# Kernel optimization log

Measured on AMD Instinct MI355X. Metric: run time of the kernel, lower is better.

The kernel has to match this reference:

```python
import jax, jax.numpy as jnp
import numpy as np

B, CI, CO = 16, 16, 16
M1, M2, M3 = 6, 6, 6
NT, NX, NY = 39, 28, 28
NXr, NYr = 14, 14  # int((n-1)/2 + 1) for n=28


def setup_inputs() -> dict:
    key = jax.random.key(0)
    ks = jax.random.split(key, 9)
    scale = 1.0 / (CI * CO)
    u = lambda k, s: scale * jax.random.uniform(k, s, dtype=jnp.float32)
    return {
        "x": jax.random.normal(ks[0], (B, CI, NT, NXr, NYr), dtype=jnp.float32),
        "wp1_re": u(ks[1], (CI, CO, M1)), "wp1_im": u(ks[2], (CI, CO, M1)),
        "wp2_re": u(ks[3], (CI, CO, M2)), "wp2_im": u(ks[4], (CI, CO, M2)),
        "wp3_re": u(ks[5], (CI, CO, M3)), "wp3_im": u(ks[6], (CI, CO, M3)),
        "wr_re": u(ks[7], (CI, CO, M1, M2, M3)), "wr_im": u(ks[8], (CI, CO, M1, M2, M3)),
    }


def _forward(x, wp1, wp2, wp3, wr):
    # grids (match torch.linspace with hardcoded nt/nx/ny and truncation)
    tt_np = np.linspace(0.0, NT - 1, NT)
    tx_np = np.linspace(0.0, 1.0, NX)[:NXr]
    ty_np = np.linspace(0.0, 1.0, NY)[:NYr]
    dtt = float(tt_np[1] - tt_np[0])
    dtx = float(tx_np[1] - tx_np[0])
    dty = float(ty_np[1] - ty_np[0])

    alpha = jnp.fft.fftn(x, axes=(-3, -2, -1))  # [B, CI, NT, NXr, NYr] complex64

    lam1 = (2j * np.pi * jnp.fft.fftfreq(NT, dtt)).astype(jnp.complex64)   # [NT]
    lam2 = (2j * np.pi * jnp.fft.fftfreq(NXr, dtx)).astype(jnp.complex64)  # [NXr]
    lam3 = (2j * np.pi * jnp.fft.fftfreq(NYr, dty)).astype(jnp.complex64)  # [NYr]

    # per-axis pole reciprocals: 1/((l1-p1)(l2-p2)(l3-p3)) = (1/(l1-p1))(1/(l2-p2))(1/(l3-p3))
    r1 = 1.0 / (lam1[:, None, None, None] - wp1[None])  # [NT,  CI, CO, M1]
    r2 = 1.0 / (lam2[:, None, None, None] - wp2[None])  # [NXr, CI, CO, M2]
    r3 = 1.0 / (lam3[:, None, None, None] - wp3[None])  # [NYr, CI, CO, M3]

    # Hw[m,n,l,i,k,p,q,r] = wr[i,k,p,q,r]*r1[m,i,k,p]*r2[n,i,k,q]*r3[l,i,k,r]
    # output_residue1[b,k,m,n,l] = sum_{i,p,q,r} alpha[b,i,m,n,l] * Hw
    or1 = jnp.einsum('bimnl,ikpqr,mikp,nikq,likr->bkmnl', alpha, wr, r1, r2, r3)
    # output_residue2[b,k,p,q,r] = -sum_{i,m,n,l} alpha[b,i,m,n,l] * Hw
    or2 = -jnp.einsum('bimnl,ikpqr,mikp,nikq,likr->bkpqr', alpha, wr, r1, r2, r3)

    x1 = jnp.real(jnp.fft.ifftn(or1, s=(NT, NXr, NYr), axes=(-3, -2, -1))).astype(jnp.float32)

    tt = jnp.asarray(tt_np, dtype=jnp.float32).astype(jnp.complex64)
    tx = jnp.asarray(tx_np, dtype=jnp.float32).astype(jnp.complex64)
    ty = jnp.asarray(ty_np, dtype=jnp.float32).astype(jnp.complex64)

    e1 = jnp.exp(wp1[..., None] * tt)  # [CI, CO, M1, NT]
    e2 = jnp.exp(wp2[..., None] * tx)  # [CI, CO, M2, NXr]
    e3 = jnp.exp(wp3[..., None] * ty)  # [CI, CO, M3, NYr]

    # x2[k,i,z,x,y] = Re( sum_{b,p,q,m} or2[k,b,p,q,m]*e1[b,i,p,z]*e2[b,i,q,x]*e3[b,i,m,y] )
    x2 = jnp.real(jnp.einsum('kbpqm,bipz,biqx,bimy->kizxy', or2, e1, e2, e3)).astype(jnp.float32)
    x2 = x2 / (NT * NXr * NYr)
    return x1 + x2


def reference(x, wp1_re, wp1_im, wp2_re, wp2_im, wp3_re, wp3_im, wr_re, wr_im):
    wp1 = jax.lax.complex(wp1_re, wp1_im)
    wp2 = jax.lax.complex(wp2_re, wp2_im)
    wp3 = jax.lax.complex(wp3_re, wp3_im)
    wr = jax.lax.complex(wr_re, wr_im)
    return _forward(x, wp1, wp2, wp3, wr)
```

## Files before the change

### kernel.cpp

```cpp
#include <hip/hip_runtime.h>

constexpr int kB  = 16;
constexpr int kC  = 16;
constexpr int kM  = 6;
constexpr int kNT = 39;
constexpr int kNX = 14;
constexpr int kNY = 14;
constexpr int kNS = kNX * kNY;
constexpr int kNF = kNT * kNS;
constexpr int kNIK = kC * kC;
constexpr int kMR = kM * kM * kM;
constexpr int kFCH = 6;

__device__ __forceinline__ float2 cmul(float2 a, float2 b) {
    return make_float2(a.x * b.x - a.y * b.y, a.x * b.y + a.y * b.x);
}
__device__ __forceinline__ void cfma(float2& c, float2 a, float2 b) {
    c.x = fmaf(a.x, b.x, fmaf(-a.y, b.y, c.x));
    c.y = fmaf(a.x, b.y, fmaf(a.y, b.x, c.y));
}

__global__ __launch_bounds__(256) void k_init(
    const float* __restrict__ wp1_re, const float* __restrict__ wp1_im,
    const float* __restrict__ wp2_re, const float* __restrict__ wp2_im,
    const float* __restrict__ wp3_re, const float* __restrict__ wp3_im,
    float2* __restrict__ F39, float2* __restrict__ F14,
    float2* __restrict__ r1t, float2* __restrict__ r2t, float2* __restrict__ r3t,
    float2* __restrict__ e1t, float2* __restrict__ e2t, float2* __restrict__ e3t)
{
    const float PI2 = 6.283185307179586f;
    int tid = blockIdx.x * blockDim.x + threadIdx.x;
    int nth = gridDim.x * blockDim.x;

    for (int idx = tid; idx < kNT * kNT; idx += nth) {
        int m = idx / kNT, t = idx % kNT;
        float ang = -PI2 * (float)((m * t) % kNT) / (float)kNT;
        float s, c; sincosf(ang, &s, &c);
        F39[idx] = make_float2(c, s);
    }
    for (int idx = tid; idx < kNX * kNX; idx += nth) {
        int a = idx / kNX, b = idx % kNX;
        float ang = -PI2 * (float)((a * b) % kNX) / (float)kNX;
        float s, c; sincosf(ang, &s, &c);
        F14[idx] = make_float2(c, s);
    }
    for (int idx = tid; idx < kNIK * kM * kNT; idx += nth) {
        int z = idx % kNT; int ikp = idx / kNT;
        float wre = wp1_re[ikp], wim = wp1_im[ikp];
        float f = (z < 20 ? (float)z : (float)(z - kNT)) / (float)kNT;
        float w = PI2 * f;
        float dr = -wre, di = w - wim;
        float inv = 1.0f / (dr * dr + di * di);
        r1t[idx] = make_float2(dr * inv, -di * inv);
        float tt = (float)z;
        float er = expf(wre * tt);
        float s, c; sincosf(wim * tt, &s, &c);
        e1t[idx] = make_float2(er * c, er * s);
    }
    for (int idx = tid; idx < kNIK * kM * kNX; idx += nth) {
        int n = idx % kNX; int ikq = idx / kNX;
        float f = (n <= 6 ? (float)n : (float)(n - kNX)) * 27.0f / 14.0f;
        float w = PI2 * f;
        float tx = (float)n * (1.0f / 27.0f);
        {
            float wre = wp2_re[ikq], wim = wp2_im[ikq];
            float dr = -wre, di = w - wim;
            float inv = 1.0f / (dr * dr + di * di);
            r2t[idx] = make_float2(dr * inv, -di * inv);
            float er = expf(wre * tx);
            float s, c; sincosf(wim * tx, &s, &c);
            e2t[idx] = make_float2(er * c, er * s);
        }
        {
            float wre = wp3_re[ikq], wim = wp3_im[ikq];
            float dr = -wre, di = w - wim;
            float inv = 1.0f / (dr * dr + di * di);
            r3t[idx] = make_float2(dr * inv, -di * inv);
            float er = expf(wre * tx);
            float s, c; sincosf(wim * tx, &s, &c);
            e3t[idx] = make_float2(er * c, er * s);
        }
    }
}

__global__ __launch_bounds__(256) void k_dft_t_real(
    const float* __restrict__ x, const float2* __restrict__ F39, float2* __restrict__ out)
{
    int bc = blockIdx.x, mg = blockIdx.y;
    __shared__ float2 Fs[13 * kNT];
    int t = threadIdx.x;
    for (int j = t; j < 13 * kNT; j += 256)
        Fs[j] = F39[(mg * 13 + j / kNT) * kNT + (j % kNT)];
    __syncthreads();
    if (t < kNS) {
        float col[kNT];
        const float* xp = x + (size_t)bc * kNF + t;
        #pragma unroll
        for (int tt = 0; tt < kNT; ++tt) col[tt] = xp[(size_t)tt * kNS];
        for (int mi = 0; mi < 13; ++mi) {
            float2 acc = make_float2(0.f, 0.f);
            #pragma unroll
            for (int tt = 0; tt < kNT; ++tt) {
                float2 f = Fs[mi * kNT + tt];
                acc.x = fmaf(f.x, col[tt], acc.x);
                acc.y = fmaf(f.y, col[tt], acc.y);
            }
            out[((size_t)bc * kNT + mg * 13 + mi) * kNS + t] = acc;
        }
    }
}

__global__ __launch_bounds__(256) void k_idft_t(
    const float2* __restrict__ in, const float2* __restrict__ F39, float2* __restrict__ out)
{
    int bk = blockIdx.x, zg = blockIdx.y;
    __shared__ float2 Fs[13 * kNT];
    int t = threadIdx.x;
    for (int j = t; j < 13 * kNT; j += 256) {
        float2 f = F39[(zg * 13 + j / kNT) * kNT + (j % kNT)];
        f.y = -f.y;
        Fs[j] = f;
    }
    __syncthreads();
    if (t < kNS) {
        float2 col[kNT];
        const float2* ip = in + (size_t)bk * kNF + t;
        #pragma unroll
        for (int m = 0; m < kNT; ++m) col[m] = ip[(size_t)m * kNS];
        for (int zi = 0; zi < 13; ++zi) {
            float2 acc = make_float2(0.f, 0.f);
            #pragma unroll
            for (int m = 0; m < kNT; ++m) cfma(acc, Fs[zi * kNT + m], col[m]);
            out[((size_t)bk * kNT + zg * 13 + zi) * kNS + t] = acc;
        }
    }
}

__global__ __launch_bounds__(256) void k_dft_xy(
    const float2* __restrict__ in, const float2* __restrict__ F14, float2* __restrict__ out)
{
    int bm = blockIdx.x;
    __shared__ float2 tile[kNS];
    __shared__ float2 tmp[kNS];
    __shared__ float2 Fs[kNX * kNX];
    int t = threadIdx.x;
    if (t < kNS) tile[t] = in[(size_t)bm * kNS + t];
    if (t < kNX * kNX) Fs[t] = F14[t];
    __syncthreads();
    if (t < kNS) {
        int n2 = t / kNY, l = t % kNY;
        float2 acc = make_float2(0.f, 0.f);
        #pragma unroll
        for (int n = 0; n < kNX; ++n) cfma(acc, Fs[n2 * kNX + n], tile[n * kNY + l]);
        tmp[t] = acc;
    }
    __syncthreads();
    if (t < kNS) {
        int n = t / kNY, l2 = t % kNY;
        float2 acc = make_float2(0.f, 0.f);
        #pragma unroll
        for (int l = 0; l < kNY; ++l) cfma(acc, Fs[l2 * kNY + l], tmp[n * kNY + l]);
        out[(size_t)bm * kNS + t] = acc;
    }
}

__global__ __launch_bounds__(256) void k_idft_xy_final(
    const float2* __restrict__ in, const float2* __restrict__ F14, float* __restrict__ outp)
{
    int bm = blockIdx.x;
    __shared__ float2 tile[kNS];
    __shared__ float2 tmp[kNS];
    __shared__ float2 Fs[kNX * kNX];
    int t = threadIdx.x;
    if (t < kNS) tile[t] = in[(size_t)bm * kNS + t];
    if (t < kNX * kNX) { float2 f = F14[t]; f.y = -f.y; Fs[t] = f; }
    __syncthreads();
    if (t < kNS) {
        int n2 = t / kNY, l = t % kNY;
        float2 acc = make_float2(0.f, 0.f);
        #pragma unroll
        for (int n = 0; n < kNX; ++n) cfma(acc, Fs[n2 * kNX + n], tile[n * kNY + l]);
        tmp[t] = acc;
    }
    __syncthreads();
    if (t < kNS) {
        int n = t / kNY, l2 = t % kNY;
        float2 acc = make_float2(0.f, 0.f);
        #pragma unroll
        for (int l = 0; l < kNY; ++l) cfma(acc, Fs[l2 * kNY + l], tmp[n * kNY + l]);
        outp[(size_t)bm * kNS + t] += acc.x * (1.0f / 7644.0f);
    }
}

__global__ __launch_bounds__(256) void k_H(
    const float* __restrict__ wr_re, const float* __restrict__ wr_im,
    const float2* __restrict__ r1t, const float2* __restrict__ r2t,
    const float2* __restrict__ r3t, float2* __restrict__ H)
{
    int ik = blockIdx.x;
    __shared__ float2 wrs[kMR];
    __shared__ float2 r1s[kM * kNT];
    __shared__ float2 r2s[kM * kNX];
    __shared__ float2 r3s[kM * kNY];
    __shared__ float2 As[kM * kM * kNY];
    __shared__ float2 Ss[kM * kNS];
    int t = threadIdx.x;
    for (int j = t; j < kMR; j += 256)
        wrs[j] = make_float2(wr_re[ik * kMR + j], wr_im[ik * kMR + j]);
    for (int j = t; j < kM * kNT; j += 256) r1s[j] = r1t[(size_t)ik * kM * kNT + j];
    for (int j = t; j < kM * kNX; j += 256) r2s[j] = r2t[(size_t)ik * kM * kNX + j];
    for (int j = t; j < kM * kNY; j += 256) r3s[j] = r3t[(size_t)ik * kM * kNY + j];
    __syncthreads();
    for (int j = t; j < kM * kM * kNY; j += 256) {
        int l = j % kNY; int pq = j / kNY;
        float2 acc = make_float2(0.f, 0.f);
        #pragma unroll
        for (int r = 0; r < kM; ++r) cfma(acc, wrs[pq * kM + r], r3s[r * kNY + l]);
        As[j] = acc;
    }
    __syncthreads();
    for (int j = t; j < kM * kNS; j += 256) {
        int l = j % kNY; int n = (j / kNY) % kNX; int p = j / kNS;
        float2 acc = make_float2(0.f, 0.f);
        #pragma unroll
        for (int q = 0; q < kM; ++q) cfma(acc, r2s[q * kNX + n], As[(p * kM + q) * kNY + l]);
        Ss[j] = acc;
    }
    __syncthreads();
    for (int j = t; j < kNF; j += 256) {
        int m = j / kNS; int nl = j % kNS;
        float2 acc = make_float2(0.f, 0.f);
        #pragma unroll
        for (int p = 0; p < kM; ++p) cfma(acc, r1s[p * kNT + m], Ss[p * kNS + nl]);
        H[(size_t)ik * kNF + j] = acc;
    }
}

__global__ __launch_bounds__(256) void k_or1(
    const float2* __restrict__ alpha, const float2* __restrict__ H, float2* __restrict__ out)
{
    int f0 = blockIdx.x * kFCH;
    __shared__ float2 As[256 * 7 + 16];
    __shared__ float2 Hs[256 * 7 + 16];
    int t = threadIdx.x;
    {
        const float2* ap = alpha + (size_t)t * kNF + f0;
        const float2* hp = H + (size_t)t * kNF + f0;
        int base = t * 7 + (t >> 4);
        #pragma unroll
        for (int j = 0; j < kFCH; ++j) {
            As[base + j] = ap[j];
            Hs[base + j] = hp[j];
        }
    }
    __syncthreads();
    int b = t >> 4, k = t & 15;
    float2 acc[kFCH];
    #pragma unroll
    for (int j = 0; j < kFCH; ++j) acc[j] = make_float2(0.f, 0.f);
    #pragma unroll
    for (int i = 0; i < kC; ++i) {
        int ai = (b * 16 + i) * 7 + b;
        int hi = (i * 16 + k) * 7 + i;
        #pragma unroll
        for (int j = 0; j < kFCH; ++j) cfma(acc[j], As[ai + j], Hs[hi + j]);
    }
    float2* op = out + (size_t)t * kNF + f0;
    #pragma unroll
    for (int j = 0; j < kFCH; ++j) op[j] = acc[j];
}

__global__ __launch_bounds__(256) void k_or2p(
    const float2* __restrict__ alpha,
    const float* __restrict__ wr_re, const float* __restrict__ wr_im,
    const float2* __restrict__ r1t, const float2* __restrict__ r2t,
    const float2* __restrict__ r3t, float2* __restrict__ P)
{
    int blk = blockIdx.x;
    int i = blk % kC; int rest = blk / kC;
    int k = rest % kC; int pb = rest / kC;
    int b0 = 2 * pb, b1 = 2 * pb + 1;
    int ik = i * kC + k;
    __shared__ float2 r1s[kM * kNT];
    __shared__ float2 r2s[kM * kNX];
    __shared__ float2 r3s[kM * kNY];
    __shared__ float2 wrs[kMR];
    __shared__ float2 T1a[kM * kNS];
    __shared__ float2 T1b[kM * kNS];
    __shared__ float2 T2a[kM * kM * kNY];
    __shared__ float2 T2b[kM * kM * kNY];
    int t = threadIdx.x;
    for (int j = t; j < kM * kNT; j += 256) r1s[j] = r1t[(size_t)ik * kM * kNT + j];
    for (int j = t; j < kM * kNX; j += 256) r2s[j] = r2t[(size_t)ik * kM * kNX + j];
    for (int j = t; j < kM * kNY; j += 256) r3s[j] = r3t[(size_t)ik * kM * kNY + j];
    for (int j = t; j < kMR; j += 256)
        wrs[j] = make_float2(wr_re[ik * kMR + j], wr_im[ik * kMR + j]);
    __syncthreads();
    if (t < kNS) {
        float2 c0 = make_float2(0.f, 0.f), c1 = c0, c2 = c0, c3 = c0, c4 = c0, c5 = c0;
        float2 d0 = c0, d1 = c0, d2 = c0, d3 = c0, d4 = c0, d5 = c0;
        const float2* ap0 = alpha + (size_t)(b0 * kC + i) * kNF + t;
        const float2* ap1 = alpha + (size_t)(b1 * kC + i) * kNF + t;
        for (int m = 0; m < kNT; ++m) {
            float2 a0 = ap0[(size_t)m * kNS];
            float2 a1 = ap1[(size_t)m * kNS];
            float2 r;
            r = r1s[0 * kNT + m]; cfma(c0, a0, r); cfma(d0, a1, r);
            r = r1s[1 * kNT + m]; cfma(c1, a0, r); cfma(d1, a1, r);
            r = r1s[2 * kNT + m]; cfma(c2, a0, r); cfma(d2, a1, r);
            r = r1s[3 * kNT + m]; cfma(c3, a0, r); cfma(d3, a1, r);
            r = r1s[4 * kNT + m]; cfma(c4, a0, r); cfma(d4, a1, r);
            r = r1s[5 * kNT + m]; cfma(c5, a0, r); cfma(d5, a1, r);
        }
        T1a[0 * kNS + t] = c0; T1a[1 * kNS + t] = c1; T1a[2 * kNS + t] = c2;
        T1a[3 * kNS + t] = c3; T1a[4 * kNS + t] = c4; T1a[5 * kNS + t] = c5;
        T1b[0 * kNS + t] = d0; T1b[1 * kNS + t] = d1; T1b[2 * kNS + t] = d2;
        T1b[3 * kNS + t] = d3; T1b[4 * kNS + t] = d4; T1b[5 * kNS + t] = d5;
    }
    __syncthreads();
    for (int j = t; j < kM * kM * kNY; j += 256) {
        int l = j % kNY; int q = (j / kNY) % kM; int p = j / (kNY * kM);
        float2 a2 = make_float2(0.f, 0.f);
        float2 b2 = make_float2(0.f, 0.f);
        #pragma unroll
        for (int n = 0; n < kNX; ++n) {
            float2 r = r2s[q * kNX + n];
            cfma(a2, T1a[p * kNS + n * kNY + l], r);
            cfma(b2, T1b[p * kNS + n * kNY + l], r);
        }
        T2a[j] = a2;
        T2b[j] = b2;
    }
    __syncthreads();
    if (t < kMR) {
        int r = t % kM; int q = (t / kM) % kM; int p = t / (kM * kM);
        float2 t3a = make_float2(0.f, 0.f);
        float2 t3b = make_float2(0.f, 0.f);
        #pragma unroll
        for (int l = 0; l < kNY; ++l) {
            float2 rr = r3s[r * kNY + l];
            cfma(t3a, T2a[(p * kM + q) * kNY + l], rr);
            cfma(t3b, T2b[(p * kM + q) * kNY + l], rr);
        }
        float2 w = wrs[t];
        P[((size_t)(b0 * kC + k) * kC + i) * kMR + t] = cmul(w, t3a);
        P[((size_t)(b1 * kC + k) * kC + i) * kMR + t] = cmul(w, t3b);
    }
}

__global__ __launch_bounds__(256) void k_or2red(
    const float2* __restrict__ P, float2* __restrict__ or2)
{
    int id = blockIdx.x * blockDim.x + threadIdx.x;
    if (id >= kB * kC * kMR) return;
    int t = id % kMR; int bk = id / kMR;
    float2 s = make_float2(0.f, 0.f);
    #pragma unroll
    for (int i = 0; i < kC; ++i) {
        float2 v = P[((size_t)bk * kC + i) * kMR + t];
        s.x += v.x; s.y += v.y;
    }
    or2[id] = make_float2(-s.x, -s.y);
}

__global__ __launch_bounds__(256) void k_x2f(
    const float2* __restrict__ or2,
    const float2* __restrict__ e1t, const float2* __restrict__ e2t,
    const float2* __restrict__ e3t, float* __restrict__ outp)
{
    int bx = blockIdx.x;
    int k = bx & 15, b = bx >> 4;
    __shared__ float2 o2s[kC * kMR];
    __shared__ float2 e1s[kC * kM * kNT];
    __shared__ float2 e2a[kC * kM * kNX];
    __shared__ float2 e3a[kC * kM * kNY];
    __shared__ float2 UsD[2][kM * kM * kNY];
    int t = threadIdx.x;
    int xx = t / kNY, yy = t % kNY;

    for (int j = t; j < kC * kMR; j += 256) {
        int c = j / kMR, u = j % kMR;
        o2s[j] = or2[(size_t)(b * kC + c) * kMR + u];
    }
    for (int j = t; j < kC * kM * kNT; j += 256) {
        int c = j / (kM * kNT), r = j % (kM * kNT);
        e1s[j] = e1t[(size_t)(c * kC + k) * (kM * kNT) + r];
    }
    for (int j = t; j < kC * kM * kNX; j += 256) {
        int c = j / (kM * kNX), r = j % (kM * kNX);
        e2a[j] = e2t[(size_t)(c * kC + k) * (kM * kNX) + r];
    }
    for (int j = t; j < kC * kM * kNY; j += 256) {
        int c = j / (kM * kNY), r = j % (kM * kNY);
        e3a[j] = e3t[(size_t)(c * kC + k) * (kM * kNY) + r];
    }
    __syncthreads();

    for (int j = t; j < kM * kM * kNY; j += 256) {
        int y = j % kNY; int pq = j / kNY;
        float2 u = make_float2(0.f, 0.f);
        #pragma unroll
        for (int m = 0; m < kM; ++m)
            cfma(u, o2s[pq * kM + m], e3a[m * kNY + y]);
        UsD[0][j] = u;
    }
    __syncthreads();

    float accz[kNT];
    #pragma unroll
    for (int z = 0; z < kNT; ++z) accz[z] = 0.f;

    for (int c = 0; c < kC; ++c) {
        int cur = c & 1;
        if (c < kC - 1) {
            int cn = c + 1;
            for (int j = t; j < kM * kM * kNY; j += 256) {
                int y = j % kNY; int pq = j / kNY;
                float2 u = make_float2(0.f, 0.f);
                #pragma unroll
                for (int m = 0; m < kM; ++m)
                    cfma(u, o2s[cn * kMR + pq * kM + m], e3a[cn * (kM * kNY) + m * kNY + y]);
                UsD[cur ^ 1][j] = u;
            }
        }
        if (t < kNS) {
            float2 e2r[kM];
            #pragma unroll
            for (int q = 0; q < kM; ++q) e2r[q] = e2a[c * (kM * kNX) + q * kNX + xx];
            #pragma unroll
            for (int p = 0; p < kM; ++p) {
                float2 v = make_float2(0.f, 0.f);
                #pragma unroll
                for (int q = 0; q < kM; ++q)
                    cfma(v, UsD[cur][(p * kM + q) * kNY + yy], e2r[q]);
                const int e1base = (c * kM + p) * kNT;
                #pragma unroll
                for (int z = 0; z < kNT; ++z) {
                    float2 e = e1s[e1base + z];
                    accz[z] = fmaf(v.x, e.x, fmaf(-v.y, e.y, accz[z]));
                }
            }
        }
        __syncthreads();
    }

    if (t < kNS) {
        const float sc = 1.0f / 7644.0f;
        size_t base = (size_t)bx * kNF + t;
        #pragma unroll
        for (int z = 0; z < kNT; ++z)
            outp[base + (size_t)z * kNS] = accz[z] * sc;
    }
}

extern "C" void kernel_launch(void* const* d_in, const int* in_sizes, int n_in,
                              void* d_out, int out_size, void* d_ws, size_t ws_size,
                              hipStream_t stream) {
    (void)in_sizes; (void)n_in; (void)out_size; (void)ws_size;
    const float* x      = (const float*)d_in[0];
    const float* wp1_re = (const float*)d_in[1];
    const float* wp1_im = (const float*)d_in[2];
    const float* wp2_re = (const float*)d_in[3];
    const float* wp2_im = (const float*)d_in[4];
    const float* wp3_re = (const float*)d_in[5];
    const float* wp3_im = (const float*)d_in[6];
    const float* wr_re  = (const float*)d_in[7];
    const float* wr_im  = (const float*)d_in[8];
    float* out = (float*)d_out;

    const size_t big = (size_t)kNIK * kNF;
    float2* A   = (float2*)d_ws;
    float2* Bb  = A + big;
    float2* Cc  = Bb + big;
    float2* OR2 = Cc + big;
    float2* r1t = OR2 + (size_t)kB * kC * kMR;
    float2* r2t = r1t + (size_t)kNIK * kM * kNT;
    float2* r3t = r2t + (size_t)kNIK * kM * kNX;
    float2* e1t = r3t + (size_t)kNIK * kM * kNY;
    float2* e2t = e1t + (size_t)kNIK * kM * kNT;
    float2* e3t = e2t + (size_t)kNIK * kM * kNX;
    float2* F39 = e3t + (size_t)kNIK * kM * kNY;
    float2* F14 = F39 + kNT * kNT;

    k_init<<<64, 256, 0, stream>>>(wp1_re, wp1_im, wp2_re, wp2_im, wp3_re, wp3_im,
                                   F39, F14, r1t, r2t, r3t, e1t, e2t, e3t);
    k_dft_t_real<<<dim3(kNIK, 3), 256, 0, stream>>>(x, F39, A);
    k_dft_xy<<<kNIK * kNT, 256, 0, stream>>>(A, F14, Bb);
    k_H<<<kNIK, 256, 0, stream>>>(wr_re, wr_im, r1t, r2t, r3t, Cc);
    k_or1<<<kNF / kFCH, 256, 0, stream>>>(Bb, Cc, A);
    k_or2p<<<(kB / 2) * kC * kC, 256, 0, stream>>>(Bb, wr_re, wr_im, r1t, r2t, r3t, Cc);
    k_or2red<<<(kB * kC * kMR + 255) / 256, 256, 0, stream>>>(Cc, OR2);
    k_x2f<<<kB * kC, 256, 0, stream>>>(OR2, e1t, e2t, e3t, out);
    k_idft_t<<<dim3(kB * kC, 3), 256, 0, stream>>>(A, F39, Cc);
    k_idft_xy_final<<<kNIK * kNT, 256, 0, stream>>>(Cc, F14, out);
}
```

Measured before the change: 207.0 us.

## Retile x2 kernel so all threads share z-axis accumulation work

The x2 kernel is rewritten so all 256 threads take part in the z-accumulation, not just the 196 spatial threads. Each thread now owns a 4x10 register tile over (spatial, z). The per-channel V intermediate is precomputed into a double-buffered shared array, and e1 is padded to 40 entries. This is meant to improve thread utilisation and cut per-thread register pressure from 39 accumulators. In exchange it adds an extra pass over shared memory and another barrier per channel.

```diff
diff --git a/kernel.cpp b/kernel.cpp
--- a/kernel.cpp
+++ b/kernel.cpp
@@ -363,7 +363,7 @@
     or2[id] = make_float2(-s.x, -s.y);
 }
 
-__global__ __launch_bounds__(256) void k_x2f(
+__global__ __launch_bounds__(256) void k_x2g(
     const float2* __restrict__ or2,
     const float2* __restrict__ e1t, const float2* __restrict__ e2t,
     const float2* __restrict__ e3t, float* __restrict__ outp)
@@ -371,12 +371,14 @@
     int bx = blockIdx.x;
     int k = bx & 15, b = bx >> 4;
     __shared__ float2 o2s[kC * kMR];
-    __shared__ float2 e1s[kC * kM * kNT];
+    __shared__ float2 e1s[kC * kM * 40];
     __shared__ float2 e2a[kC * kM * kNX];
     __shared__ float2 e3a[kC * kM * kNY];
-    __shared__ float2 UsD[2][kM * kM * kNY];
-    int t = threadIdx.x;
-    int xx = t / kNY, yy = t % kNY;
+    __shared__ float2 Us[kM * kM * kNY];
+    __shared__ float2 Vb[2][kM * 200];
+    int t = threadIdx.x;
+    int sl = t & 63;
+    int zt = t >> 6;
 
     for (int j = t; j < kC * kMR; j += 256) {
         int c = j / kMR, u = j % kMR;
@@ -384,8 +386,11 @@
     }
     for (int j = t; j < kC * kM * kNT; j += 256) {
         int c = j / (kM * kNT), r = j % (kM * kNT);
-        e1s[j] = e1t[(size_t)(c * kC + k) * (kM * kNT) + r];
-    }
+        int p = r / kNT, z = r % kNT;
+        e1s[(c * kM + p) * 40 + z] = e1t[(size_t)(c * kC + k) * (kM * kNT) + r];
+    }
+    for (int j = t; j < kC * kM; j += 256)
+        e1s[j * 40 + 39] = make_float2(0.f, 0.f);
     for (int j = t; j < kC * kM * kNX; j += 256) {
         int c = j / (kM * kNX), r = j % (kM * kNX);
         e2a[j] = e2t[(size_t)(c * kC + k) * (kM * kNX) + r];
@@ -397,59 +402,93 @@
     __syncthreads();
 
     for (int j = t; j < kM * kM * kNY; j += 256) {
-        int y = j % kNY; int pq = j / kNY;
+        int y = j % kNY, pq = j / kNY;
         float2 u = make_float2(0.f, 0.f);
         #pragma unroll
         for (int m = 0; m < kM; ++m)
             cfma(u, o2s[pq * kM + m], e3a[m * kNY + y]);
-        UsD[0][j] = u;
-    }
-    __syncthreads();
-
-    float accz[kNT];
+        Us[j] = u;
+    }
+    __syncthreads();
+    for (int j = t; j < kM * 200; j += 256) {
+        int p = j / 200, s = j % 200;
+        float2 v = make_float2(0.f, 0.f);
+        if (s < kNS) {
+            int x = s / kNY, y = s % kNY;
+            #pragma unroll
+            for (int q = 0; q < kM; ++q)
+                cfma(v, Us[(p * kM + q) * kNY + y], e2a[q * kNX + x]);
+        }
+        Vb[0][j] = v;
+    }
+    __syncthreads();
+
+    float accz[10][4];
     #pragma unroll
-    for (int z = 0; z < kNT; ++z) accz[z] = 0.f;
+    for (int zi = 0; zi < 10; ++zi)
+        #pragma unroll
+        for (int j = 0; j < 4; ++j) accz[zi][j] = 0.f;
 
     for (int c = 0; c < kC; ++c) {
         int cur = c & 1;
-        if (c < kC - 1) {
+        if (c + 1 < kC) {
             int cn = c + 1;
             for (int j = t; j < kM * kM * kNY; j += 256) {
-                int y = j % kNY; int pq = j / kNY;
+                int y = j % kNY, pq = j / kNY;
                 float2 u = make_float2(0.f, 0.f);
                 #pragma unroll
                 for (int m = 0; m < kM; ++m)
-                    cfma(u, o2s[cn * kMR + pq * kM + m], e3a[cn * (kM * kNY) + m * kNY + y]);
-                UsD[cur ^ 1][j] = u;
+                    cfma(u, o2s[cn * kMR + pq * kM + m],
+                            e3a[cn * (kM * kNY) + m * kNY + y]);
+                Us[j] = u;
             }
         }
-        if (t < kNS) {
-            float2 e2r[kM];
+        #pragma unroll
+        for (int p = 0; p < kM; ++p) {
+            float2 vr[4];
             #pragma unroll
-            for (int q = 0; q < kM; ++q) e2r[q] = e2a[c * (kM * kNX) + q * kNX + xx];
+            for (int j = 0; j < 4; ++j) vr[j] = Vb[cur][p * 200 + sl + 64 * j];
+            const int e1base = (c * kM + p) * 40 + zt;
             #pragma unroll
-            for (int p = 0; p < kM; ++p) {
+            for (int zi = 0; zi < 10; ++zi) {
+                float2 e = e1s[e1base + 4 * zi];
+                #pragma unroll
+                for (int j = 0; j < 4; ++j)
+                    accz[zi][j] = fmaf(vr[j].x, e.x, fmaf(-vr[j].y, e.y, accz[zi][j]));
+            }
+        }
+        __syncthreads();
+        if (c + 1 < kC) {
+            int cn = c + 1;
+            for (int j = t; j < kM * 200; j += 256) {
+                int p = j / 200, s = j % 200;
                 float2 v = make_float2(0.f, 0.f);
-                #pragma unroll
-                for (int q = 0; q < kM; ++q)
-                    cfma(v, UsD[cur][(p * kM + q) * kNY + yy], e2r[q]);
-                const int e1base = (c * kM + p) * kNT;
-                #pragma unroll
-                for (int z = 0; z < kNT; ++z) {
-                    float2 e = e1s[e1base + z];
-                    accz[z] = fmaf(v.x, e.x, fmaf(-v.y, e.y, accz[z]));
+                if (s < kNS) {
+                    int x = s / kNY, y = s % kNY;
+                    #pragma unroll
+                    for (int q = 0; q < kM; ++q)
+                        cfma(v, Us[(p * kM + q) * kNY + y],
+                                e2a[cn * (kM * kNX) + q * kNX + x]);
                 }
+                Vb[cur ^ 1][j] = v;
             }
         }
         __syncthreads();
     }
 
-    if (t < kNS) {
-        const float sc = 1.0f / 7644.0f;
-        size_t base = (size_t)bx * kNF + t;
-        #pragma unroll
-        for (int z = 0; z < kNT; ++z)
-            outp[base + (size_t)z * kNS] = accz[z] * sc;
+    const float sc = 1.0f / 7644.0f;
+    size_t base = (size_t)bx * kNF;
+    #pragma unroll
+    for (int zi = 0; zi < 10; ++zi) {
+        int z = zt + 4 * zi;
+        if (z < kNT) {
+            #pragma unroll
+            for (int j = 0; j < 4; ++j) {
+                int s = sl + 64 * j;
+                if (s < kNS)
+                    outp[base + (size_t)z * kNS + s] = accz[zi][j] * sc;
+            }
+        }
     }
 }
 
@@ -490,7 +529,7 @@
     k_or1<<<kNF / kFCH, 256, 0, stream>>>(Bb, Cc, A);
     k_or2p<<<(kB / 2) * kC * kC, 256, 0, stream>>>(Bb, wr_re, wr_im, r1t, r2t, r3t, Cc);
     k_or2red<<<(kB * kC * kMR + 255) / 256, 256, 0, stream>>>(Cc, OR2);
-    k_x2f<<<kB * kC, 256, 0, stream>>>(OR2, e1t, e2t, e3t, out);
+    k_x2g<<<kB * kC, 256, 0, stream>>>(OR2, e1t, e2t, e3t, out);
     k_idft_t<<<dim3(kB * kC, 3), 256, 0, stream>>>(A, F39, Cc);
     k_idft_xy_final<<<kNIK * kNT, 256, 0, stream>>>(Cc, F14, out);
 }
```

After: 202.3 us. 1.02x faster.

## Split x2 stage into parallel V-build and register-tiled z-contraction GEMM

Applied to the files above, without the earlier changes.

The single k_x2f kernel, which launched only 256 blocks and ran the channel loop serially, is replaced by two kernels. The first builds the intermediate V[b,k,c,p,s] in global workspace with one block per (b,k,c). The second contracts V over (c,p) against e1 in a 4x4 register-tiled GEMM, split over three z-chunks. The work runs in two batch halves so V fits in the reused workspace buffer A, which is free after idft_t. This aims to raise parallelism and reuse at the cost of extra global memory traffic and more launches.

```diff
diff --git a/kernel.cpp b/kernel.cpp
--- a/kernel.cpp
+++ b/kernel.cpp
@@ -11,6 +11,7 @@
 constexpr int kNIK = kC * kC;
 constexpr int kMR = kM * kM * kM;
 constexpr int kFCH = 6;
+constexpr int kVS = 256;
 
 __device__ __forceinline__ float2 cmul(float2 a, float2 b) {
     return make_float2(a.x * b.x - a.y * b.y, a.x * b.y + a.y * b.x);
@@ -363,93 +364,102 @@
     or2[id] = make_float2(-s.x, -s.y);
 }
 
-__global__ __launch_bounds__(256) void k_x2f(
+__global__ __launch_bounds__(256) void k_x2v(
     const float2* __restrict__ or2,
-    const float2* __restrict__ e1t, const float2* __restrict__ e2t,
-    const float2* __restrict__ e3t, float* __restrict__ outp)
+    const float2* __restrict__ e2t, const float2* __restrict__ e3t,
+    float2* __restrict__ Vg, int pb)
+{
+    int bid = blockIdx.x;
+    int c = bid & 15; int rest = bid >> 4;
+    int k = rest & 15; int bh = rest >> 4;
+    int b = pb * 8 + bh;
+    int ck = c * kC + k;
+    __shared__ float2 o2s[kMR];
+    __shared__ float2 e2s[kM * kNX];
+    __shared__ float2 e3s[kM * kNY];
+    __shared__ float2 Us[kM * kM * kNY];
+    int t = threadIdx.x;
+    if (t < kMR) o2s[t] = or2[(size_t)(b * kC + c) * kMR + t];
+    if (t < kM * kNX) e2s[t] = e2t[(size_t)ck * (kM * kNX) + t];
+    if (t < kM * kNY) e3s[t] = e3t[(size_t)ck * (kM * kNY) + t];
+    __syncthreads();
+    for (int j = t; j < kM * kM * kNY; j += 256) {
+        int y = j % kNY, pq = j / kNY;
+        float2 u = make_float2(0.f, 0.f);
+        #pragma unroll
+        for (int m = 0; m < kM; ++m) cfma(u, o2s[pq * kM + m], e3s[m * kNY + y]);
+        Us[j] = u;
+    }
+    __syncthreads();
+    size_t vbase = ((size_t)(bh * kC + k) * (kC * kM) + c * kM) * kVS;
+    for (int j = t; j < kM * kVS; j += 256) {
+        int p = j >> 8, s = j & 255;
+        float2 v = make_float2(0.f, 0.f);
+        if (s < kNS) {
+            int x = s / kNY, y = s % kNY;
+            #pragma unroll
+            for (int q = 0; q < kM; ++q)
+                cfma(v, Us[(p * kM + q) * kNY + y], e2s[q * kNX + x]);
+        }
+        Vg[vbase + (size_t)p * kVS + s] = v;
+    }
+}
+
+__global__ __launch_bounds__(256) void k_x2gemm(
+    const float2* __restrict__ Vg, const float2* __restrict__ e1t,
+    float* __restrict__ outp, int pb)
 {
     int bx = blockIdx.x;
-    int k = bx & 15, b = bx >> 4;
-    __shared__ float2 o2s[kC * kMR];
-    __shared__ float2 e1s[kC * kM * kNT];
-    __shared__ float2 e2a[kC * kM * kNX];
-    __shared__ float2 e3a[kC * kM * kNY];
-    __shared__ float2 UsD[2][kM * kM * kNY];
-    int t = threadIdx.x;
-    int xx = t / kNY, yy = t % kNY;
-
-    for (int j = t; j < kC * kMR; j += 256) {
-        int c = j / kMR, u = j % kMR;
-        o2s[j] = or2[(size_t)(b * kC + c) * kMR + u];
-    }
-    for (int j = t; j < kC * kM * kNT; j += 256) {
-        int c = j / (kM * kNT), r = j % (kM * kNT);
-        e1s[j] = e1t[(size_t)(c * kC + k) * (kM * kNT) + r];
-    }
-    for (int j = t; j < kC * kM * kNX; j += 256) {
-        int c = j / (kM * kNX), r = j % (kM * kNX);
-        e2a[j] = e2t[(size_t)(c * kC + k) * (kM * kNX) + r];
-    }
-    for (int j = t; j < kC * kM * kNY; j += 256) {
-        int c = j / (kM * kNY), r = j % (kM * kNY);
-        e3a[j] = e3t[(size_t)(c * kC + k) * (kM * kNY) + r];
-    }
-    __syncthreads();
-
-    for (int j = t; j < kM * kM * kNY; j += 256) {
-        int y = j % kNY; int pq = j / kNY;
-        float2 u = make_float2(0.f, 0.f);
-        #pragma unroll
-        for (int m = 0; m < kM; ++m)
-            cfma(u, o2s[pq * kM + m], e3a[m * kNY + y]);
-        UsD[0][j] = u;
-    }
-    __syncthreads();
-
-    float accz[kNT];
+    int k = bx & 15, bh = bx >> 4;
+    int b = pb * 8 + bh;
+    int z0 = blockIdx.y * 13;
+    __shared__ float2 e1w[96 * 16];
+    int t = threadIdx.x;
+    for (int j = t; j < 96 * 16; j += 256) {
+        int row = j >> 4, zi = j & 15;
+        int c = row / kM, p = row % kM;
+        float2 e = make_float2(0.f, 0.f);
+        if (zi < 13)
+            e = e1t[((size_t)(c * kC + k) * kM + p) * kNT + z0 + zi];
+        e1w[j] = e;
+    }
+    __syncthreads();
+
+    int sl = t & 63, zt = t >> 6;
+    const float2* vp = Vg + (size_t)(bh * kC + k) * (kC * kM) * kVS + sl;
+    float acc[4][4];
     #pragma unroll
-    for (int z = 0; z < kNT; ++z) accz[z] = 0.f;
-
-    for (int c = 0; c < kC; ++c) {
-        int cur = c & 1;
-        if (c < kC - 1) {
-            int cn = c + 1;
-            for (int j = t; j < kM * kM * kNY; j += 256) {
-                int y = j % kNY; int pq = j / kNY;
-                float2 u = make_float2(0.f, 0.f);
-                #pragma unroll
-                for (int m = 0; m < kM; ++m)
-                    cfma(u, o2s[cn * kMR + pq * kM + m], e3a[cn * (kM * kNY) + m * kNY + y]);
-                UsD[cur ^ 1][j] = u;
+    for (int zi = 0; zi < 4; ++zi)
+        #pragma unroll
+        for (int j = 0; j < 4; ++j) acc[zi][j] = 0.f;
+
+    for (int kk = 0; kk < kC * kM; ++kk) {
+        float2 vr[4];
+        #pragma unroll
+        for (int j = 0; j < 4; ++j) vr[j] = vp[(size_t)kk * kVS + 64 * j];
+        const int e1base = kk * 16 + zt;
+        #pragma unroll
+        for (int zi = 0; zi < 4; ++zi) {
+            float2 e = e1w[e1base + 4 * zi];
+            #pragma unroll
+            for (int j = 0; j < 4; ++j)
+                acc[zi][j] = fmaf(vr[j].x, e.x, fmaf(-vr[j].y, e.y, acc[zi][j]));
+        }
+    }
+
+    const float sc = 1.0f / 7644.0f;
+    size_t base = (size_t)(b * kC + k) * kNF;
+    #pragma unroll
+    for (int zi = 0; zi < 4; ++zi) {
+        int zloc = zt + 4 * zi;
+        if (zloc < 13) {
+            size_t zb = base + (size_t)(z0 + zloc) * kNS;
+            #pragma unroll
+            for (int j = 0; j < 4; ++j) {
+                int s = sl + 64 * j;
+                if (s < kNS) outp[zb + s] = acc[zi][j] * sc;
             }
         }
-        if (t < kNS) {
-            float2 e2r[kM];
-            #pragma unroll
-            for (int q = 0; q < kM; ++q) e2r[q] = e2a[c * (kM * kNX) + q * kNX + xx];
-            #pragma unroll
-            for (int p = 0; p < kM; ++p) {
-                float2 v = make_float2(0.f, 0.f);
-                #pragma unroll
-                for (int q = 0; q < kM; ++q)
-                    cfma(v, UsD[cur][(p * kM + q) * kNY + yy], e2r[q]);
-                const int e1base = (c * kM + p) * kNT;
-                #pragma unroll
-                for (int z = 0; z < kNT; ++z) {
-                    float2 e = e1s[e1base + z];
-                    accz[z] = fmaf(v.x, e.x, fmaf(-v.y, e.y, accz[z]));
-                }
-            }
-        }
-        __syncthreads();
-    }
-
-    if (t < kNS) {
-        const float sc = 1.0f / 7644.0f;
-        size_t base = (size_t)bx * kNF + t;
-        #pragma unroll
-        for (int z = 0; z < kNT; ++z)
-            outp[base + (size_t)z * kNS] = accz[z] * sc;
     }
 }
 
@@ -481,6 +491,7 @@
     float2* e3t = e2t + (size_t)kNIK * kM * kNX;
     float2* F39 = e3t + (size_t)kNIK * kM * kNY;
     float2* F14 = F39 + kNT * kNT;
+    float2* Vg  = (float2*)d_ws;
 
     k_init<<<64, 256, 0, stream>>>(wp1_re, wp1_im, wp2_re, wp2_im, wp3_re, wp3_im,
                                    F39, F14, r1t, r2t, r3t, e1t, e2t, e3t);
@@ -490,7 +501,10 @@
     k_or1<<<kNF / kFCH, 256, 0, stream>>>(Bb, Cc, A);
     k_or2p<<<(kB / 2) * kC * kC, 256, 0, stream>>>(Bb, wr_re, wr_im, r1t, r2t, r3t, Cc);
     k_or2red<<<(kB * kC * kMR + 255) / 256, 256, 0, stream>>>(Cc, OR2);
-    k_x2f<<<kB * kC, 256, 0, stream>>>(OR2, e1t, e2t, e3t, out);
     k_idft_t<<<dim3(kB * kC, 3), 256, 0, stream>>>(A, F39, Cc);
+    for (int pb = 0; pb < 2; ++pb) {
+        k_x2v<<<8 * kC * kC, 256, 0, stream>>>(OR2, e2t, e3t, Vg, pb);
+        k_x2gemm<<<dim3(8 * kC, 3), 256, 0, stream>>>(Vg, e1t, out, pb);
+    }
     k_idft_xy_final<<<kNIK * kNT, 256, 0, stream>>>(Cc, F14, out);
 }
```

After: 228.1 us. 1.1x slower.
